# Kernel optimization log

Measured on AMD Instinct MI355X. Metric: run time of the kernel, lower is better.

The kernel has to match this reference:

```python
import jax, jax.numpy as jnp
import numpy as np

B, D, L, H, T = 256, 512, 8, 8, 71
DH = D // H
SCALE = 0.01

def _lrelu(x):
    return jax.nn.leaky_relu(x, 0.2)

def _rms(x, dims, w):
    return w * x * jax.lax.rsqrt(jnp.mean(x * x, axis=dims, keepdims=True) + 1e-6)

def _conv(x, w, b, pad):
    y = jax.lax.conv_general_dilated(x, w, (1, 1), pad, dimension_numbers=('NCHW', 'OIHW', 'NCHW'))
    return y + b[None, :, None, None]

def _mha(x, qkv, nw):
    b_, d_, t_ = x.shape
    # einsum 'bdt,nhdD->nbhtD' -> (3,B,H,T,dh)
    y = jnp.einsum('bdt,nhdD->nbhtD', _lrelu(x), qkv)
    y = _rms(y, -2, nw)  # RMSNorm over the token axis (torch dim=-2)
    q, k, v = y[0], y[1], y[2]
    attn = jax.nn.softmax(jnp.einsum('bhtd,bhTd->bhtT', q, k) / np.float32(np.sqrt(DH)), axis=-1)
    out = jnp.einsum('bhtT,bhTd->bhdt', attn, v)  # (B,H,dh,T)
    return out.reshape(b_, d_, t_)

def _convblock(x, w1, b1, w2, b2, nw):
    b_, d_, t_ = x.shape
    y = x.reshape(b_, d_, 8, 8)
    y = _conv(_lrelu(y), w1, b1, 'SAME')
    y = _rms(y, (-1, -2), nw)
    y = _conv(_lrelu(y), w2, b2, 'SAME')
    return y.reshape(b_, d_, t_)

def _forward(fen, move, rank_emb, file_emb, fen_emb, move_emb, abs_emb, ln_w, ln_b, emb_qkv, emb_norm_w, qkv, mha_norm_w, conv1_w, conv1_b, conv2_w, conv2_b, cb_norm_w, out_norm_w, co1_w, co1_b, co2_w, co2_b):
    pos = (rank_emb + file_emb).reshape(64, D)
    mv = (pos[move] + move_emb) * 0.58          # (B,2,D)
    f = fen_emb[fen]                             # (B,133,D)
    board = 0.5 * (f[:, :64] + f[:, 64:128] + pos)
    x = jnp.concatenate([board, f[:, 128:], mv], axis=1) + abs_emb  # (B,71,D)
    x = jnp.swapaxes(x, -1, -2)                  # (B,D,71)
    mu = jnp.mean(x, -1, keepdims=True)
    var = jnp.mean((x - mu) ** 2, -1, keepdims=True)
    x = (x - mu) * jax.lax.rsqrt(var + 1e-5) * ln_w + ln_b  # LayerNorm over T=71
    y = _mha(x, emb_qkv, emb_norm_w)
    x = x[:, :, :64] + y[:, :, :64]              # keep the 64 board squares
    for i in range(L):
        x = x + _convblock(x, conv1_w[i], conv1_b[i], conv2_w[i], conv2_b[i], cb_norm_w[i])
        x = x + _mha(x, qkv[i], mha_norm_w[i])
    x = x.reshape(B, D, 8, 8)
    x = _conv(_lrelu(x), co1_w, co1_b, 'SAME')
    x = _rms(x, (-1, -2), out_norm_w)
    x = _conv(_lrelu(x), co2_w, co2_b, 'VALID')  # (B,1,1,1)
    return x.reshape(-1)

def setup_inputs():
    key = jax.random.key(0)
    ks = jax.random.split(key, 16)
    n = lambda k, s, sc: jax.random.normal(k, s, dtype=jnp.float32) * sc
    return {
        'fen': jax.random.randint(ks[0], (B, 133), 0, 17),
        'move': jax.random.randint(ks[1], (B, 2), 0, 64),
        'rank_emb': n(ks[2], (8, 1, D), SCALE),
        'file_emb': n(ks[3], (1, 8, D), SCALE),
        'fen_emb': n(ks[4], (17, D), SCALE),
        'move_emb': n(ks[5], (2, D), SCALE),
        'abs_emb': n(ks[6], (71, D), SCALE),
        'ln_w': jnp.ones((71,), jnp.float32),
        'ln_b': jnp.zeros((71,), jnp.float32),
        'emb_qkv': n(ks[7], (3, H, D, DH), SCALE),
        'emb_norm_w': jnp.ones((1,), jnp.float32),
        'qkv': n(ks[8], (L, 3, H, D, DH), SCALE * 0.64),
        'mha_norm_w': jnp.ones((L, 1), jnp.float32),
        'conv1_w': n(ks[9], (L, D, D, 3, 3), SCALE * 0.64),
        'conv1_b': jnp.zeros((L, D), jnp.float32),
        'conv2_w': n(ks[10], (L, D, D, 3, 3), SCALE * 0.64),
        'conv2_b': jnp.zeros((L, D), jnp.float32),
        'cb_norm_w': jnp.ones((L, 1), jnp.float32),
        'out_norm_w': jnp.ones((1,), jnp.float32),
        'co1_w': n(ks[11], (2 * D, D, 3, 3), SCALE),
        'co1_b': jnp.zeros((2 * D,), jnp.float32),
        'co2_w': n(ks[12], (1, 2 * D, 8, 8), SCALE),
        'co2_b': jnp.zeros((1,), jnp.float32),
    }

def reference(fen, move, rank_emb, file_emb, fen_emb, move_emb, abs_emb, ln_w, ln_b, emb_qkv, emb_norm_w, qkv, mha_norm_w, conv1_w, conv1_b, conv2_w, conv2_b, cb_norm_w, out_norm_w, co1_w, co1_b, co2_w, co2_b):
    return _forward(fen, move, rank_emb, file_emb, fen_emb, move_emb, abs_emb, ln_w, ln_b, emb_qkv, emb_norm_w, qkv, mha_norm_w, conv1_w, conv1_b, conv2_w, conv2_b, cb_norm_w, out_norm_w, co1_w, co1_b, co2_w, co2_b)
```

## Files before the change

kernel.cpp:

```cpp
#include <hip/hip_runtime.h>
#include <hip/hip_bf16.h>
#include <cstdint>
#include <cstddef>


typedef float f32x4 __attribute__((ext_vector_type(4)));
typedef short short8 __attribute__((ext_vector_type(8)));

__device__ __forceinline__ float lrelu(float v) { return v > 0.f ? v : 0.2f * v; }
__device__ __forceinline__ __hip_bfloat16 tobf(float v) { return __float2bfloat16(v); }
__device__ __forceinline__ float frombf(__hip_bfloat16 v) { return __bfloat162float(v); }

__global__ __launch_bounds__(256) void repack_qkv_w0(
    const float* __restrict__ emb_qkv, __hip_bfloat16* __restrict__ Wq0)
{
  int o = blockIdx.x * 256 + threadIdx.x;
  int j = o >> 9, d = o & 511;
  int n = j >> 9, h = (j >> 6) & 7, dh = j & 63;
  Wq0[o] = tobf(emb_qkv[(((n * 8 + h) * 512 + d) << 6) + dh]);
}

__global__ __launch_bounds__(256) void repack_qkv_w2(
    const float* __restrict__ qkvw, __hip_bfloat16* __restrict__ Wq2)
{
  const int t = blockIdx.x * 256 + threadIdx.x;
  const int lane = t & 63;
  const int nj = (t >> 6) % 96;
  int rest = (t >> 6) / 96;
  const int ks = rest & 1;
  const int kc = (rest >> 1) & 7;
  const int L = rest >> 4;
  const int j = nj * 16 + (lane & 15);
  const int d0 = kc * 64 + ks * 32 + (lane >> 4) * 8;
  const int n = j >> 9, h = (j >> 6) & 7, dh = j & 63;
  const float* src = qkvw + ((((size_t)L * 3 + n) * 8 + h) * 512 + d0) * 64 + dh;
  __hip_bfloat16 tmp[8];
  #pragma unroll
  for (int e = 0; e < 8; ++e) tmp[e] = tobf(src[(size_t)e * 64]);
  *(uint4*)&Wq2[(size_t)t * 8] = *(const uint4*)tmp;
}

__global__ __launch_bounds__(256) void repack_conv_w2(
    const float* __restrict__ w, __hip_bfloat16* __restrict__ W2, int COUT)
{
  const int t = blockIdx.x * 256 + threadIdx.x;
  if (t >= (COUT << 6)) return;
  const int lr = t & 15;
  const int cbg = (t >> 4) & 63;
  const int oj = t >> 10;
  const int cc = cbg >> 3, ks = (cbg >> 2) & 1, lg = cbg & 3;
  const int o = oj * 16 + lr;
  const int NJ = COUT >> 4;
  const float* src = w + ((size_t)o * 512 + cbg * 8) * 9;
  #pragma unroll
  for (int k = 0; k < 9; ++k) {
    __hip_bfloat16 tmp[8];
    #pragma unroll
    for (int e = 0; e < 8; ++e) tmp[e] = tobf(src[e * 9 + k]);
    size_t di = ((((size_t)cc * 9 + k) * NJ + oj) * 2 + ks) * 512 + (lg * 16 + lr) * 8;
    *(uint4*)&W2[di] = *(const uint4*)tmp;
  }
}

__global__ __launch_bounds__(256) void repack_conv_pair(
    const float* __restrict__ w1, const float* __restrict__ w2s,
    __hip_bfloat16* __restrict__ WA, __hip_bfloat16* __restrict__ WB)
{
  int t = blockIdx.x * 256 + threadIdx.x;
  const float* w = (t < 32768) ? w1 : w2s;
  __hip_bfloat16* W2 = (t < 32768) ? WA : WB;
  t &= 32767;
  const int lr = t & 15;
  const int cbg = (t >> 4) & 63;
  const int oj = t >> 10;
  const int cc = cbg >> 3, ks = (cbg >> 2) & 1, lg = cbg & 3;
  const int o = oj * 16 + lr;
  const float* src = w + ((size_t)o * 512 + cbg * 8) * 9;
  #pragma unroll
  for (int k = 0; k < 9; ++k) {
    __hip_bfloat16 tmp[8];
    #pragma unroll
    for (int e = 0; e < 8; ++e) tmp[e] = tobf(src[e * 9 + k]);
    size_t di = ((((size_t)cc * 9 + k) * 32 + oj) * 2 + ks) * 512 + (lg * 16 + lr) * 8;
    *(uint4*)&W2[di] = *(const uint4*)tmp;
  }
}

__global__ __launch_bounds__(256) void build_ln_kernel(
    const int* __restrict__ fen, const int* __restrict__ move,
    const float* __restrict__ rank_emb, const float* __restrict__ file_emb,
    const float* __restrict__ fen_emb, const float* __restrict__ move_emb,
    const float* __restrict__ abs_emb, const float* __restrict__ lnw,
    const float* __restrict__ lnb, __hip_bfloat16* __restrict__ X71)
{
  const int gid = blockIdx.x * 256 + threadIdx.x;
  const int b = gid >> 9, d = gid & 511;
  const int* fb = fen + b * 133;

  float sum = 0.f, sq = 0.f, mu = 0.f, rstd = 0.f;
  #pragma unroll 1
  for (int pass = 0; pass < 2; ++pass) {
    if (pass) {
      mu = sum * (1.f / 71.f);
      float var = sq * (1.f / 71.f) - mu * mu;
      rstd = rsqrtf(var + 1e-5f);
    }
    #pragma unroll 1
    for (int t = 0; t < 71; ++t) {
      float a = abs_emb[t * 512 + d];
      float v;
      if (t < 64) {
        float pos = rank_emb[(t >> 3) * 512 + d] + file_emb[(t & 7) * 512 + d];
        v = 0.5f * (fen_emb[fb[t] * 512 + d] + fen_emb[fb[64 + t] * 512 + d] + pos) + a;
      } else if (t < 69) {
        v = fen_emb[fb[t + 64] * 512 + d] + a;
      } else {
        int j = t - 69;
        int s = move[b * 2 + j];
        float pos = rank_emb[(s >> 3) * 512 + d] + file_emb[(s & 7) * 512 + d];
        v = (pos + move_emb[j * 512 + d]) * 0.58f + a;
      }
      if (pass) X71[(size_t)gid * 71 + t] = tobf((v - mu) * rstd * lnw[t] + lnb[t]);
      else { sum += v; sq += v * v; }
    }
  }
}

template <int T, int TP>
__global__ __launch_bounds__(256) void proj71_kernel(
    const __hip_bfloat16* __restrict__ xin, const __hip_bfloat16* __restrict__ Wq,
    const float* __restrict__ nw,
    __hip_bfloat16* __restrict__ qk, __hip_bfloat16* __restrict__ vT)
{
  const int b  = blockIdx.x / 6;
  const int jb = (blockIdx.x % 6) * 256;
  const int tid = threadIdx.x;
  const int lane = tid & 63, wv = tid >> 6;
  const int lr = lane & 15, lg = lane >> 4;

  __shared__ __hip_bfloat16 xt[TP * 72];
  __shared__ __hip_bfloat16 wl[256 * 72];

  constexpr int MI = TP / 16;
  f32x4 acc[MI][4];
  #pragma unroll
  for (int mi = 0; mi < MI; ++mi)
    #pragma unroll
    for (int ni = 0; ni < 4; ++ni) acc[mi][ni] = {0.f, 0.f, 0.f, 0.f};

  for (int c0 = 0; c0 < 512; c0 += 64) {
    for (int i = tid; i < 64 * TP; i += 256) {
      int d = i / TP, t = i - d * TP;
      float v = (t < T) ? lrelu(frombf(xin[((size_t)(b * 512 + c0 + d)) * T + t])) : 0.f;
      xt[t * 72 + d] = tobf(v);
    }
    for (int i = tid; i < 2048; i += 256) {
      int j = i >> 3, cb = i & 7;
      *(uint4*)&wl[j * 72 + cb * 8] =
          *(const uint4*)&Wq[(size_t)(jb + j) * 512 + c0 + cb * 8];
    }
    __syncthreads();
    #pragma unroll
    for (int ks = 0; ks < 2; ++ks) {
      short8 a[MI], bb[4];
      #pragma unroll
      for (int mi = 0; mi < MI; ++mi)
        a[mi] = *(const short8*)&xt[(mi * 16 + lr) * 72 + ks * 32 + lg * 8];
      #pragma unroll
      for (int ni = 0; ni < 4; ++ni)
        bb[ni] = *(const short8*)&wl[(wv * 64 + ni * 16 + lr) * 72 + ks * 32 + lg * 8];
      #pragma unroll
      for (int mi = 0; mi < MI; ++mi)
        #pragma unroll
        for (int ni = 0; ni < 4; ++ni)
          acc[mi][ni] = __builtin_amdgcn_mfma_f32_16x16x32_bf16(
              a[mi], bb[ni], acc[mi][ni], 0, 0, 0);
    }
    __syncthreads();
  }

  #pragma unroll
  for (int ni = 0; ni < 4; ++ni) {
    const int j = jb + wv * 64 + ni * 16 + lr;
    float ss = 0.f;
    #pragma unroll
    for (int mi = 0; mi < MI; ++mi)
      #pragma unroll
      for (int r = 0; r < 4; ++r) ss += acc[mi][ni][r] * acc[mi][ni][r];
    ss += __shfl_xor(ss, 16);
    ss += __shfl_xor(ss, 32);
    const float sc = nw[0] * rsqrtf(ss * (1.f / T) + 1e-6f);
    if (j < 1024) {
      #pragma unroll
      for (int mi = 0; mi < MI; ++mi)
        #pragma unroll
        for (int r = 0; r < 4; ++r) {
          int t = mi * 16 + lg * 4 + r;
          if (t < T)
            qk[((size_t)b * T + t) * 1024 + j] = tobf(acc[mi][ni][r] * sc);
        }
    } else {
      const int jj = j - 1024;
      #pragma unroll
      for (int mi = 0; mi < MI; ++mi)
        #pragma unroll
        for (int r = 0; r < 4; ++r) {
          int t = mi * 16 + lg * 4 + r;
          vT[((size_t)b * 512 + jj) * TP + t] = tobf(acc[mi][ni][r] * sc);
        }
    }
  }
}

__global__ __launch_bounds__(256) void proj64_kernel(
    const float* __restrict__ x,
    const __hip_bfloat16* __restrict__ Wq2,
    const float* __restrict__ nw,
    __hip_bfloat16* __restrict__ qk, __hip_bfloat16* __restrict__ vT)
{
  const int b    = blockIdx.x / 6;
  const int jseg = blockIdx.x % 6;
  const int tid = threadIdx.x;
  const int lane = tid & 63, wv = tid >> 6;
  const int lr = lane & 15, lg = lane >> 4;

  __shared__ __hip_bfloat16 xt[2][64 * 72];

  f32x4 acc[4][4];
  #pragma unroll
  for (int mi = 0; mi < 4; ++mi)
    #pragma unroll
    for (int ni = 0; ni < 4; ++ni) acc[mi][ni] = {0.f, 0.f, 0.f, 0.f};

  f32x4 sreg[4];
  const int s_d  = tid >> 4;
  const int s_t4 = (tid & 15) << 2;

  #define PSTAGE_LOAD(kc_)                                                    \
    {                                                                         \
      const float* xb_ = x + ((size_t)b * 512 + (kc_) * 64 + s_d) * 64 + s_t4; \
      _Pragma("unroll")                                                       \
      for (int u = 0; u < 4; ++u) sreg[u] = *(const f32x4*)&xb_[u * 1024];    \
    }
  #define PSTAGE_WRITE(buf_)                                                  \
    {                                                                         \
      _Pragma("unroll")                                                       \
      for (int u = 0; u < 4; ++u) {                                           \
        _Pragma("unroll")                                                     \
        for (int j = 0; j < 4; ++j)                                           \
          xt[buf_][(s_t4 + j) * 72 + s_d + u * 16] = tobf(lrelu(sreg[u][j])); \
      }                                                                       \
    }

  PSTAGE_LOAD(0);
  PSTAGE_WRITE(0);
  __syncthreads();

  const int njb0 = jseg * 16 + wv * 4;

  for (int kc = 0; kc < 8; ++kc) {
    const int cur = kc & 1;
    if (kc < 7) PSTAGE_LOAD(kc + 1);
    const __hip_bfloat16* xb = xt[cur];
    #pragma unroll
    for (int ks = 0; ks < 2; ++ks) {
      short8 bv[4], av[4];
      #pragma unroll
      for (int ni = 0; ni < 4; ++ni)
        bv[ni] = *(const short8*)
            &Wq2[((((size_t)kc * 2 + ks) * 96) + njb0 + ni) * 512 + lane * 8];
      #pragma unroll
      for (int mi = 0; mi < 4; ++mi)
        av[mi] = *(const short8*)&xb[(mi * 16 + lr) * 72 + ks * 32 + lg * 8];
      #pragma unroll
      for (int mi = 0; mi < 4; ++mi)
        #pragma unroll
        for (int ni = 0; ni < 4; ++ni)
          acc[mi][ni] = __builtin_amdgcn_mfma_f32_16x16x32_bf16(
              av[mi], bv[ni], acc[mi][ni], 0, 0, 0);
    }
    if (kc < 7) PSTAGE_WRITE(cur ^ 1);
    __syncthreads();
  }
  #undef PSTAGE_LOAD
  #undef PSTAGE_WRITE

  #pragma unroll
  for (int ni = 0; ni < 4; ++ni) {
    const int j = jseg * 256 + wv * 64 + ni * 16 + lr;
    float ss = 0.f;
    #pragma unroll
    for (int mi = 0; mi < 4; ++mi)
      #pragma unroll
      for (int r = 0; r < 4; ++r) ss += acc[mi][ni][r] * acc[mi][ni][r];
    ss += __shfl_xor(ss, 16);
    ss += __shfl_xor(ss, 32);
    const float sc = nw[0] * rsqrtf(ss * (1.f / 64.f) + 1e-6f);
    if (j < 1024) {
      #pragma unroll
      for (int mi = 0; mi < 4; ++mi)
        #pragma unroll
        for (int r = 0; r < 4; ++r) {
          int t = mi * 16 + lg * 4 + r;
          qk[((size_t)b * 64 + t) * 1024 + j] = tobf(acc[mi][ni][r] * sc);
        }
    } else {
      const int jj = j - 1024;
      #pragma unroll
      for (int mi = 0; mi < 4; ++mi)
        #pragma unroll
        for (int r = 0; r < 4; ++r) {
          int t = mi * 16 + lg * 4 + r;
          vT[((size_t)b * 512 + jj) * 64 + t] = tobf(acc[mi][ni][r] * sc);
        }
    }
  }
}

template <int T, bool RESBF, bool WRITEXC>
__global__ __launch_bounds__(256) void attn2_kernel(
    const __hip_bfloat16* __restrict__ qk,
    const __hip_bfloat16* __restrict__ vT,
    const void* __restrict__ res, float* __restrict__ out,
    __hip_bfloat16* __restrict__ xcout)
{
  constexpr int TP = (T == 71) ? 80 : 64;
  constexpr int TK = (T + 31) / 32;
  constexpr int RS = 72;
  constexpr int PS = TK * 32 + 8;
  constexpr int KR = (T == 71) ? 80 : 64;
  constexpr int SC = (T == 71) ? 82 : 66;
  constexpr int NCF = KR / 16;
  constexpr int NFW = (NCF + 3) / 4;
  constexpr int RANGE = (TK * 32) / 4;

  constexpr int Q_OFF = 0;
  constexpr int K_OFF = Q_OFF + 64 * RS * 2;
  constexpr int V_OFF = K_OFF + KR * RS * 2;
  constexpr int S_OFF = V_OFF + 64 * PS * 2;
  constexpr int BYTES = S_OFF + 64 * SC * 4;
  __shared__ __align__(16) char smem[BYTES];
  __hip_bfloat16* qs = (__hip_bfloat16*)(smem + Q_OFF);
  __hip_bfloat16* ksh = (__hip_bfloat16*)(smem + K_OFF);
  __hip_bfloat16* vs = (__hip_bfloat16*)(smem + V_OFF);
  float* ss = (float*)(smem + S_OFF);
  __hip_bfloat16* ps = (__hip_bfloat16*)(smem + S_OFF);

  const int b = blockIdx.x >> 3, h = blockIdx.x & 7;
  const int tid = threadIdx.x;
  const int lane = tid & 63, wv = tid >> 6;
  const int lr = lane & 15, lg = lane >> 4;

  for (int i = tid; i < BYTES / 16; i += 256) ((uint4*)smem)[i] = uint4{0, 0, 0, 0};
  __syncthreads();

  const __hip_bfloat16* qb = qk + (size_t)b * T * 1024 + h * 64;
  for (int v = tid; v < 512; v += 256) {
    int t = v >> 3, d0 = (v & 7) * 8;
    *(uint4*)&qs[t * RS + d0] = *(const uint4*)&qb[(size_t)t * 1024 + d0];
  }
  for (int v = tid; v < T * 8; v += 256) {
    int t = v >> 3, d0 = (v & 7) * 8;
    *(uint4*)&ksh[t * RS + d0] = *(const uint4*)&qb[(size_t)t * 1024 + 512 + d0];
  }
  constexpr int VV = TP / 8;
  for (int v = tid; v < 64 * VV; v += 256) {
    int dh = v / VV, tc = (v - dh * VV) * 8;
    *(uint4*)&vs[dh * PS + tc] =
        *(const uint4*)&vT[((size_t)b * 512 + h * 64 + dh) * TP + tc];
  }
  __syncthreads();

  f32x4 sacc[NFW][4];
  #pragma unroll
  for (int fi = 0; fi < NFW; ++fi)
    #pragma unroll
    for (int mi = 0; mi < 4; ++mi) sacc[fi][mi] = {0.f, 0.f, 0.f, 0.f};
  #pragma unroll
  for (int ks2 = 0; ks2 < 2; ++ks2) {
    short8 a[4];
    #pragma unroll
    for (int mi = 0; mi < 4; ++mi)
      a[mi] = *(const short8*)&qs[(mi * 16 + lr) * RS + ks2 * 32 + lg * 8];
    #pragma unroll
    for (int fi = 0; fi < NFW; ++fi) {
      const int f = wv + fi * 4;
      if (f < NCF) {
        short8 bb = *(const short8*)&ksh[(f * 16 + lr) * RS + ks2 * 32 + lg * 8];
        #pragma unroll
        for (int mi = 0; mi < 4; ++mi)
          sacc[fi][mi] = __builtin_amdgcn_mfma_f32_16x16x32_bf16(
              a[mi], bb, sacc[fi][mi], 0, 0, 0);
      }
    }
  }
  #pragma unroll
  for (int fi = 0; fi < NFW; ++fi) {
    const int f = wv + fi * 4;
    if (f < NCF) {
      #pragma unroll
      for (int mi = 0; mi < 4; ++mi)
        #pragma unroll
        for (int r = 0; r < 4; ++r)
          ss[(mi * 16 + lg * 4 + r) * SC + f * 16 + lr] = sacc[fi][mi][r] * 0.125f;
    }
  }
  __syncthreads();

  {
    const int row = tid >> 2, q4 = tid & 3;
    float sv[RANGE];
    float mx = -3.0e38f;
    #pragma unroll
    for (int i = 0; i < RANGE; ++i) {
      int c = q4 * RANGE + i;
      sv[i] = (c < T) ? ss[row * SC + c] : -3.0e38f;
      mx = fmaxf(mx, sv[i]);
    }
    mx = fmaxf(mx, __shfl_xor(mx, 1));
    mx = fmaxf(mx, __shfl_xor(mx, 2));
    float sm = 0.f;
    #pragma unroll
    for (int i = 0; i < RANGE; ++i) {
      int c = q4 * RANGE + i;
      sv[i] = (c < T) ? __expf(sv[i] - mx) : 0.f;
      sm += sv[i];
    }
    sm += __shfl_xor(sm, 1);
    sm += __shfl_xor(sm, 2);
    const float inv = 1.f / sm;
    __syncthreads();
    #pragma unroll
    for (int i = 0; i < RANGE; ++i)
      ps[row * PS + q4 * RANGE + i] = tobf(sv[i] * inv);
  }
  __syncthreads();

  f32x4 oacc[4];
  #pragma unroll
  for (int mi = 0; mi < 4; ++mi) oacc[mi] = {0.f, 0.f, 0.f, 0.f};
  #pragma unroll
  for (int ks2 = 0; ks2 < TK; ++ks2) {
    short8 bb = *(const short8*)&vs[(wv * 16 + lr) * PS + ks2 * 32 + lg * 8];
    #pragma unroll
    for (int mi = 0; mi < 4; ++mi) {
      short8 a = *(const short8*)&ps[(mi * 16 + lr) * PS + ks2 * 32 + lg * 8];
      oacc[mi] = __builtin_amdgcn_mfma_f32_16x16x32_bf16(a, bb, oacc[mi], 0, 0, 0);
    }
  }

  const int dh = wv * 16 + lr;
  const size_t chb = (size_t)b * 512 + h * 64 + dh;
  #pragma unroll
  for (int mi = 0; mi < 4; ++mi) {
    const int t0 = mi * 16 + lg * 4;
    const size_t idx = chb * 64 + t0;
    f32x4 v = oacc[mi];
    if constexpr (RESBF) {
      const __hip_bfloat16* rb = (const __hip_bfloat16*)res + chb * T + t0;
      #pragma unroll
      for (int r = 0; r < 4; ++r) v[r] += frombf(rb[r]);
    } else {
      v += *(const f32x4*)&((const float*)res)[idx];
    }
    *(f32x4*)&out[idx] = v;
    if constexpr (WRITEXC) {
      #pragma unroll
      for (int r = 0; r < 4; ++r)
        xcout[((size_t)b * 64 + t0 + r) * 512 + (h << 6) + dh] = tobf(lrelu(v[r]));
    }
  }
}

template <bool RMSOUT, bool RESADD, bool INBF, bool OUTBF>
__global__ __launch_bounds__(256) void conv_mfma2b(
    const void* __restrict__ xin,
    const __hip_bfloat16* __restrict__ W2,
    const float* __restrict__ bias,
    const float* __restrict__ nw,
    const float* __restrict__ res,
    void* __restrict__ outp,
    int COUT)
{
  const int ntc = COUT >> 8;
  const int b = blockIdx.x / ntc;
  const int nt = blockIdx.x - b * ntc;
  const int o0 = nt << 8;
  const int NJ = COUT >> 4;
  const int tid = threadIdx.x;
  const int lane = tid & 63, wv = tid >> 6;
  const int lr = lane & 15, lg = lane >> 4;

  __shared__ __hip_bfloat16 xt[2][100 * 72];

  f32x4 acc[4][4];
  #pragma unroll
  for (int mi = 0; mi < 4; ++mi)
    #pragma unroll
    for (int ni = 0; ni < 4; ++ni) acc[mi][ni] = {0.f, 0.f, 0.f, 0.f};

  for (int i = tid; i < 7200; i += 256) { xt[0][i] = tobf(0.f); xt[1][i] = tobf(0.f); }

  f32x4 sreg[4];
  const int s_ci = tid >> 4;
  const int s_p4 = (tid & 15) << 2;
  const int s_row = (((s_p4 >> 3) + 1) * 10 + (s_p4 & 7) + 1) * 72;
  uint4 sregb[2];
  const int c_cg = tid & 7;
  const int c_cell0 = tid >> 3;
  const int c_lofs0 = (((c_cell0 >> 3) + 1) * 10 + (c_cell0 & 7) + 1) * 72 + c_cg * 8;
  const int c_cell1 = c_cell0 + 32;
  const int c_lofs1 = (((c_cell1 >> 3) + 1) * 10 + (c_cell1 & 7) + 1) * 72 + c_cg * 8;

  auto stage_load = [&](int cc_) {
    if constexpr (INBF) {
      const __hip_bfloat16* xbf = (const __hip_bfloat16*)xin;
      const __hip_bfloat16* p0 =
          xbf + ((size_t)b * 64 + c_cell0) * 512 + cc_ * 64 + c_cg * 8;
      sregb[0] = *(const uint4*)p0;
      sregb[1] = *(const uint4*)(p0 + 32 * 512);
    } else {
      const float* xf = (const float*)xin;
      const float* xb_ = xf + ((size_t)b * 512 + cc_ * 64 + s_ci) * 64 + s_p4;
      #pragma unroll
      for (int u = 0; u < 4; ++u) sreg[u] = *(const f32x4*)&xb_[u * 1024];
    }
  };
  auto stage_write = [&](int buf_) {
    if constexpr (INBF) {
      *(uint4*)&xt[buf_][c_lofs0] = sregb[0];
      *(uint4*)&xt[buf_][c_lofs1] = sregb[1];
    } else {
      #pragma unroll
      for (int u = 0; u < 4; ++u)
        #pragma unroll
        for (int j = 0; j < 4; ++j)
          xt[buf_][s_row + j * 72 + s_ci + u * 16] = tobf(lrelu(sreg[u][j]));
    }
  };

  stage_load(0);
  __syncthreads();
  stage_write(0);
  __syncthreads();

  const int ojb2 = ((o0 >> 4) + wv * 4) * 2;

  for (int cc = 0; cc < 8; ++cc) {
    const int cur = cc & 1;
    if (cc < 7) stage_load(cc + 1);
    const __hip_bfloat16* xb = xt[cur];

    #pragma unroll
    for (int k = 0; k < 9; ++k) {
      const int dy = k / 3 - 1, dx = k - (k / 3) * 3 - 1;
      const int ii0 = (lr >> 3) + dy + 1;
      const int jj0 = (lr & 7) + dx + 1;
      const size_t slab = ((size_t)(cc * 9 + k) * NJ) * 2 + ojb2;
      short8 bv[2][4], av[2][4];
      #pragma unroll
      for (int ni = 0; ni < 4; ++ni)
        #pragma unroll
        for (int ks = 0; ks < 2; ++ks)
          bv[ks][ni] = *(const short8*)&W2[(slab + ni * 2 + ks) * 512 + lane * 8];
      #pragma unroll
      for (int ks = 0; ks < 2; ++ks)
        #pragma unroll
        for (int mi = 0; mi < 4; ++mi)
          av[ks][mi] = *(const short8*)&xb[((ii0 + mi * 2) * 10 + jj0) * 72 + ks * 32 + lg * 8];
      #pragma unroll
      for (int ks = 0; ks < 2; ++ks)
        #pragma unroll
        for (int mi = 0; mi < 4; ++mi)
          #pragma unroll
          for (int ni = 0; ni < 4; ++ni)
            acc[mi][ni] = __builtin_amdgcn_mfma_f32_16x16x32_bf16(
                av[ks][mi], bv[ks][ni], acc[mi][ni], 0, 0, 0);
    }
    if (cc < 7) stage_write(cur ^ 1);
    __syncthreads();
  }

  #pragma unroll
  for (int ni = 0; ni < 4; ++ni) {
    const int o = o0 + wv * 64 + ni * 16 + lr;
    const float bvs = bias[o];
    float sc = 1.f;
    if constexpr (RMSOUT) {
      float ssq = 0.f;
      #pragma unroll
      for (int mi = 0; mi < 4; ++mi)
        #pragma unroll
        for (int r = 0; r < 4; ++r) {
          float v = acc[mi][ni][r] + bvs;
          ssq += v * v;
        }
      ssq += __shfl_xor(ssq, 16);
      ssq += __shfl_xor(ssq, 32);
      sc = nw[0] * rsqrtf(ssq * (1.f / 64.f) + 1e-6f);
    }
    if constexpr (OUTBF) {
      __hip_bfloat16* tc = (__hip_bfloat16*)outp;
      #pragma unroll
      for (int mi = 0; mi < 4; ++mi)
        #pragma unroll
        for (int r = 0; r < 4; ++r) {
          int cell = mi * 16 + lg * 4 + r;
          tc[((size_t)b * 64 + cell) * COUT + o] =
              tobf(lrelu((acc[mi][ni][r] + bvs) * sc));
        }
    } else {
      float* outf = (float*)outp;
      #pragma unroll
      for (int mi = 0; mi < 4; ++mi) {
        size_t idx = ((size_t)b * COUT + o) * 64 + mi * 16 + lg * 4;
        f32x4 v;
        #pragma unroll
        for (int r = 0; r < 4; ++r) v[r] = (acc[mi][ni][r] + bvs) * sc;
        if constexpr (RESADD) v += *(const f32x4*)&res[idx];
        *(f32x4*)&outf[idx] = v;
      }
    }
  }
}

__global__ __launch_bounds__(256) void co2_kernel(
    const float* __restrict__ xf, const float* __restrict__ w,
    const float* __restrict__ cb, float* __restrict__ out)
{
  const int b = blockIdx.x, tid = threadIdx.x;
  const float* xb = xf + (size_t)b * 65536;
  float acc = 0.f;
  for (int i = tid; i < 65536; i += 256)
    acc += lrelu(xb[i]) * w[i];
  #pragma unroll
  for (int off = 32; off; off >>= 1) acc += __shfl_down(acc, off);
  __shared__ float red[4];
  if ((tid & 63) == 0) red[tid >> 6] = acc;
  __syncthreads();
  if (tid == 0) out[b] = red[0] + red[1] + red[2] + red[3] + cb[0];
}

extern "C" void kernel_launch(void* const* d_in, const int* in_sizes, int n_in,
                              void* d_out, int out_size, void* d_ws, size_t ws_size,
                              hipStream_t stream)
{
  const int*   fen        = (const int*)d_in[0];
  const int*   move       = (const int*)d_in[1];
  const float* rank_emb   = (const float*)d_in[2];
  const float* file_emb   = (const float*)d_in[3];
  const float* fen_emb    = (const float*)d_in[4];
  const float* move_emb   = (const float*)d_in[5];
  const float* abs_emb    = (const float*)d_in[6];
  const float* ln_w       = (const float*)d_in[7];
  const float* ln_b       = (const float*)d_in[8];
  const float* emb_qkv    = (const float*)d_in[9];
  const float* emb_norm_w = (const float*)d_in[10];
  const float* qkvw_in    = (const float*)d_in[11];
  const float* mha_norm_w = (const float*)d_in[12];
  const float* conv1_w    = (const float*)d_in[13];
  const float* conv1_b    = (const float*)d_in[14];
  const float* conv2_w    = (const float*)d_in[15];
  const float* conv2_b    = (const float*)d_in[16];
  const float* cb_norm_w  = (const float*)d_in[17];
  const float* out_norm_w = (const float*)d_in[18];
  const float* co1_w      = (const float*)d_in[19];
  const float* co1_b      = (const float*)d_in[20];
  const float* co2_w      = (const float*)d_in[21];
  const float* co2_b      = (const float*)d_in[22];
  float* out = (float*)d_out;

  char* base = (char*)d_ws;
  __hip_bfloat16* X71 = (__hip_bfloat16*)base;
  float* X64 = (float*)(base + 18612224);
  char* t1b  = base + 52166656;
  __hip_bfloat16* Wq0 = (__hip_bfloat16*)(base + 119275520);
  __hip_bfloat16* Wq2 = (__hip_bfloat16*)(base + 120848384);
  __hip_bfloat16* qk71 = (__hip_bfloat16*)t1b;
  __hip_bfloat16* vT71 = (__hip_bfloat16*)(t1b + 37224448);
  __hip_bfloat16* qk64 = (__hip_bfloat16*)t1b;
  __hip_bfloat16* vT64 = (__hip_bfloat16*)(t1b + 33554432);
  __hip_bfloat16* Xc   = (__hip_bfloat16*)(t1b + 50331648);
  __hip_bfloat16* Tc   = (__hip_bfloat16*)t1b;
  float* F1 = (float*)t1b;
  __hip_bfloat16* WcA = (__hip_bfloat16*)base;
  __hip_bfloat16* WcB = (__hip_bfloat16*)(base + 4718592);

  repack_qkv_w0<<<3072, 256, 0, stream>>>(emb_qkv, Wq0);
  repack_qkv_w2<<<3072, 256, 0, stream>>>(qkvw_in, Wq2);

  build_ln_kernel<<<512, 256, 0, stream>>>(fen, move, rank_emb, file_emb,
                                           fen_emb, move_emb, abs_emb,
                                           ln_w, ln_b, X71);
  proj71_kernel<71, 80><<<1536, 256, 0, stream>>>(X71, Wq0, emb_norm_w, qk71, vT71);
  attn2_kernel<71, true, false><<<2048, 256, 0, stream>>>(qk71, vT71, X71, X64,
                                                          nullptr);

  for (int l = 0; l < 8; ++l) {
    repack_conv_pair<<<256, 256, 0, stream>>>(conv1_w + (size_t)l * 512 * 512 * 9,
                                              conv2_w + (size_t)l * 512 * 512 * 9,
                                              WcA, WcB);
    if (l == 0)
      conv_mfma2b<true, false, false, true><<<512, 256, 0, stream>>>(
          X64, WcA, conv1_b + l * 512, cb_norm_w + l, nullptr, Tc, 512);
    else
      conv_mfma2b<true, false, true, true><<<512, 256, 0, stream>>>(
          Xc, WcA, conv1_b + l * 512, cb_norm_w + l, nullptr, Tc, 512);
    conv_mfma2b<false, true, true, false><<<512, 256, 0, stream>>>(
        Tc, WcB, conv2_b + l * 512, nullptr, X64, X64, 512);
    proj64_kernel<<<1536, 256, 0, stream>>>(X64, Wq2 + (size_t)l * 786432,
                                            mha_norm_w + l, qk64, vT64);
    if (l < 7)
      attn2_kernel<64, false, true><<<2048, 256, 0, stream>>>(qk64, vT64, X64,
                                                              X64, Xc);
    else
      attn2_kernel<64, false, false><<<2048, 256, 0, stream>>>(qk64, vT64, X64,
                                                               X64, nullptr);
  }

  repack_conv_w2<<<256, 256, 0, stream>>>(co1_w, WcA, 1024);
  conv_mfma2b<true, false, false, false><<<1024, 256, 0, stream>>>(
      X64, WcA, co1_b, out_norm_w, nullptr, F1, 1024);
  co2_kernel<<<256, 256, 0, stream>>>(F1, co2_w, co2_b, out);
}
```

Measured before the change: 2.647 ms.

## Share conv weight fragments across two batches per block and unify qkv repack

The conv kernel now runs 512-thread blocks where two 256-thread halves process two batch elements with the same output-channel tile. Each half keeps its own double-buffered LDS slab, and blocks are ordered so neighbouring blocks touch the same weights, which is meant to improve weight reuse in cache. The embedding qkv weights are repacked into the same MFMA-fragment layout as the layer weights in a single kernel. The embedding projection then reads B fragments straight from global memory instead of staging them through LDS. The larger blocks use twice the LDS, which may lower occupancy.

New measurement: 2.709 ms. 1.02x slower.

```diff
diff --git a/kernel.cpp b/kernel.cpp
--- a/kernel.cpp
+++ b/kernel.cpp
@@ -11,17 +11,9 @@
 __device__ __forceinline__ __hip_bfloat16 tobf(float v) { return __float2bfloat16(v); }
 __device__ __forceinline__ float frombf(__hip_bfloat16 v) { return __bfloat162float(v); }
 
-__global__ __launch_bounds__(256) void repack_qkv_w0(
-    const float* __restrict__ emb_qkv, __hip_bfloat16* __restrict__ Wq0)
-{
-  int o = blockIdx.x * 256 + threadIdx.x;
-  int j = o >> 9, d = o & 511;
-  int n = j >> 9, h = (j >> 6) & 7, dh = j & 63;
-  Wq0[o] = tobf(emb_qkv[(((n * 8 + h) * 512 + d) << 6) + dh]);
-}
-
-__global__ __launch_bounds__(256) void repack_qkv_w2(
-    const float* __restrict__ qkvw, __hip_bfloat16* __restrict__ Wq2)
+__global__ __launch_bounds__(256) void repack_qkv_all(
+    const float* __restrict__ emb_qkv, const float* __restrict__ qkvw,
+    __hip_bfloat16* __restrict__ Wq2)
 {
   const int t = blockIdx.x * 256 + threadIdx.x;
   const int lane = t & 63;
@@ -33,7 +25,9 @@
   const int j = nj * 16 + (lane & 15);
   const int d0 = kc * 64 + ks * 32 + (lane >> 4) * 8;
   const int n = j >> 9, h = (j >> 6) & 7, dh = j & 63;
-  const float* src = qkvw + ((((size_t)L * 3 + n) * 8 + h) * 512 + d0) * 64 + dh;
+  const float* src =
+      (L == 0) ? emb_qkv + (((size_t)(n * 8 + h) * 512 + d0) << 6) + dh
+               : qkvw + ((((size_t)(L - 1) * 3 + n) * 8 + h) * 512 + d0) * 64 + dh;
   __hip_bfloat16 tmp[8];
   #pragma unroll
   for (int e = 0; e < 8; ++e) tmp[e] = tobf(src[(size_t)e * 64]);
@@ -127,19 +121,19 @@
 }
 
 template <int T, int TP>
-__global__ __launch_bounds__(256) void proj71_kernel(
-    const __hip_bfloat16* __restrict__ xin, const __hip_bfloat16* __restrict__ Wq,
+__global__ __launch_bounds__(256) void proj71b_kernel(
+    const __hip_bfloat16* __restrict__ xin,
+    const __hip_bfloat16* __restrict__ Wq2,
     const float* __restrict__ nw,
     __hip_bfloat16* __restrict__ qk, __hip_bfloat16* __restrict__ vT)
 {
-  const int b  = blockIdx.x / 6;
-  const int jb = (blockIdx.x % 6) * 256;
+  const int b    = blockIdx.x / 6;
+  const int jseg = blockIdx.x % 6;
   const int tid = threadIdx.x;
   const int lane = tid & 63, wv = tid >> 6;
   const int lr = lane & 15, lg = lane >> 4;
 
   __shared__ __hip_bfloat16 xt[TP * 72];
-  __shared__ __hip_bfloat16 wl[256 * 72];
 
   constexpr int MI = TP / 16;
   f32x4 acc[MI][4];
@@ -148,40 +142,39 @@
     #pragma unroll
     for (int ni = 0; ni < 4; ++ni) acc[mi][ni] = {0.f, 0.f, 0.f, 0.f};
 
-  for (int c0 = 0; c0 < 512; c0 += 64) {
+  const int njb0 = jseg * 16 + wv * 4;
+
+  for (int kc = 0; kc < 8; ++kc) {
+    const int c0 = kc * 64;
     for (int i = tid; i < 64 * TP; i += 256) {
       int d = i / TP, t = i - d * TP;
       float v = (t < T) ? lrelu(frombf(xin[((size_t)(b * 512 + c0 + d)) * T + t])) : 0.f;
       xt[t * 72 + d] = tobf(v);
     }
-    for (int i = tid; i < 2048; i += 256) {
-      int j = i >> 3, cb = i & 7;
-      *(uint4*)&wl[j * 72 + cb * 8] =
-          *(const uint4*)&Wq[(size_t)(jb + j) * 512 + c0 + cb * 8];
-    }
     __syncthreads();
     #pragma unroll
     for (int ks = 0; ks < 2; ++ks) {
-      short8 a[MI], bb[4];
+      short8 bv[4], av[MI];
+      #pragma unroll
+      for (int ni = 0; ni < 4; ++ni)
+        bv[ni] = *(const short8*)
+            &Wq2[((((size_t)kc * 2 + ks) * 96) + njb0 + ni) * 512 + lane * 8];
       #pragma unroll
       for (int mi = 0; mi < MI; ++mi)
-        a[mi] = *(const short8*)&xt[(mi * 16 + lr) * 72 + ks * 32 + lg * 8];
-      #pragma unroll
-      for (int ni = 0; ni < 4; ++ni)
-        bb[ni] = *(const short8*)&wl[(wv * 64 + ni * 16 + lr) * 72 + ks * 32 + lg * 8];
+        av[mi] = *(const short8*)&xt[(mi * 16 + lr) * 72 + ks * 32 + lg * 8];
       #pragma unroll
       for (int mi = 0; mi < MI; ++mi)
         #pragma unroll
         for (int ni = 0; ni < 4; ++ni)
           acc[mi][ni] = __builtin_amdgcn_mfma_f32_16x16x32_bf16(
-              a[mi], bb[ni], acc[mi][ni], 0, 0, 0);
+              av[mi], bv[ni], acc[mi][ni], 0, 0, 0);
     }
     __syncthreads();
   }
 
   #pragma unroll
   for (int ni = 0; ni < 4; ++ni) {
-    const int j = jb + wv * 64 + ni * 16 + lr;
+    const int j = jseg * 256 + wv * 64 + ni * 16 + lr;
     float ss = 0.f;
     #pragma unroll
     for (int mi = 0; mi < MI; ++mi)
@@ -473,7 +466,7 @@
 }
 
 template <bool RMSOUT, bool RESADD, bool INBF, bool OUTBF>
-__global__ __launch_bounds__(256) void conv_mfma2b(
+__global__ __launch_bounds__(512) void conv_mfma2c(
     const void* __restrict__ xin,
     const __hip_bfloat16* __restrict__ W2,
     const float* __restrict__ bias,
@@ -483,15 +476,20 @@
     int COUT)
 {
   const int ntc = COUT >> 8;
-  const int b = blockIdx.x / ntc;
-  const int nt = blockIdx.x - b * ntc;
+  const int lpn = 8 / ntc;
+  const int g = blockIdx.x >> 3, s = blockIdx.x & 7;
+  const int nt = s / lpn;
+  const int bp = g * lpn + (s % lpn);
   const int o0 = nt << 8;
   const int NJ = COUT >> 4;
   const int tid = threadIdx.x;
-  const int lane = tid & 63, wv = tid >> 6;
+  const int bg = tid >> 8;
+  const int t256 = tid & 255;
+  const int b = bp * 2 + bg;
+  const int lane = tid & 63, wv = (t256 >> 6);
   const int lr = lane & 15, lg = lane >> 4;
 
-  __shared__ __hip_bfloat16 xt[2][100 * 72];
+  __shared__ __hip_bfloat16 xt[2][2][100 * 72];
 
   f32x4 acc[4][4];
   #pragma unroll
@@ -499,15 +497,15 @@
     #pragma unroll
     for (int ni = 0; ni < 4; ++ni) acc[mi][ni] = {0.f, 0.f, 0.f, 0.f};
 
-  for (int i = tid; i < 7200; i += 256) { xt[0][i] = tobf(0.f); xt[1][i] = tobf(0.f); }
+  for (int i = tid; i < 3600; i += 512) ((uint4*)xt)[i] = uint4{0, 0, 0, 0};
 
   f32x4 sreg[4];
-  const int s_ci = tid >> 4;
-  const int s_p4 = (tid & 15) << 2;
+  const int s_ci = t256 >> 4;
+  const int s_p4 = (t256 & 15) << 2;
   const int s_row = (((s_p4 >> 3) + 1) * 10 + (s_p4 & 7) + 1) * 72;
   uint4 sregb[2];
-  const int c_cg = tid & 7;
-  const int c_cell0 = tid >> 3;
+  const int c_cg = t256 & 7;
+  const int c_cell0 = t256 >> 3;
   const int c_lofs0 = (((c_cell0 >> 3) + 1) * 10 + (c_cell0 & 7) + 1) * 72 + c_cg * 8;
   const int c_cell1 = c_cell0 + 32;
   const int c_lofs1 = (((c_cell1 >> 3) + 1) * 10 + (c_cell1 & 7) + 1) * 72 + c_cg * 8;
@@ -528,14 +526,14 @@
   };
   auto stage_write = [&](int buf_) {
     if constexpr (INBF) {
-      *(uint4*)&xt[buf_][c_lofs0] = sregb[0];
-      *(uint4*)&xt[buf_][c_lofs1] = sregb[1];
+      *(uint4*)&xt[buf_][bg][c_lofs0] = sregb[0];
+      *(uint4*)&xt[buf_][bg][c_lofs1] = sregb[1];
     } else {
       #pragma unroll
       for (int u = 0; u < 4; ++u)
         #pragma unroll
         for (int j = 0; j < 4; ++j)
-          xt[buf_][s_row + j * 72 + s_ci + u * 16] = tobf(lrelu(sreg[u][j]));
+          xt[buf_][bg][s_row + j * 72 + s_ci + u * 16] = tobf(lrelu(sreg[u][j]));
     }
   };
 
@@ -549,7 +547,7 @@
   for (int cc = 0; cc < 8; ++cc) {
     const int cur = cc & 1;
     if (cc < 7) stage_load(cc + 1);
-    const __hip_bfloat16* xb = xt[cur];
+    const __hip_bfloat16* xb = xt[cur][bg];
 
     #pragma unroll
     for (int k = 0; k < 9; ++k) {
@@ -674,8 +672,7 @@
   __hip_bfloat16* X71 = (__hip_bfloat16*)base;
   float* X64 = (float*)(base + 18612224);
   char* t1b  = base + 52166656;
-  __hip_bfloat16* Wq0 = (__hip_bfloat16*)(base + 119275520);
-  __hip_bfloat16* Wq2 = (__hip_bfloat16*)(base + 120848384);
+  __hip_bfloat16* Wq2 = (__hip_bfloat16*)(base + 119275520);
   __hip_bfloat16* qk71 = (__hip_bfloat16*)t1b;
   __hip_bfloat16* vT71 = (__hip_bfloat16*)(t1b + 37224448);
   __hip_bfloat16* qk64 = (__hip_bfloat16*)t1b;
@@ -686,13 +683,13 @@
   __hip_bfloat16* WcA = (__hip_bfloat16*)base;
   __hip_bfloat16* WcB = (__hip_bfloat16*)(base + 4718592);
 
-  repack_qkv_w0<<<3072, 256, 0, stream>>>(emb_qkv, Wq0);
-  repack_qkv_w2<<<3072, 256, 0, stream>>>(qkvw_in, Wq2);
+  repack_qkv_all<<<3456, 256, 0, stream>>>(emb_qkv, qkvw_in, Wq2);
 
   build_ln_kernel<<<512, 256, 0, stream>>>(fen, move, rank_emb, file_emb,
                                            fen_emb, move_emb, abs_emb,
                                            ln_w, ln_b, X71);
-  proj71_kernel<71, 80><<<1536, 256, 0, stream>>>(X71, Wq0, emb_norm_w, qk71, vT71);
+  proj71b_kernel<71, 80><<<1536, 256, 0, stream>>>(X71, Wq2, emb_norm_w,
+                                                   qk71, vT71);
   attn2_kernel<71, true, false><<<2048, 256, 0, stream>>>(qk71, vT71, X71, X64,
                                                           nullptr);
 
@@ -701,14 +698,14 @@
                                               conv2_w + (size_t)l * 512 * 512 * 9,
                                               WcA, WcB);
     if (l == 0)
-      conv_mfma2b<true, false, false, true><<<512, 256, 0, stream>>>(
+      conv_mfma2c<true, false, false, true><<<256, 512, 0, stream>>>(
           X64, WcA, conv1_b + l * 512, cb_norm_w + l, nullptr, Tc, 512);
     else
-      conv_mfma2b<true, false, true, true><<<512, 256, 0, stream>>>(
+      conv_mfma2c<true, false, true, true><<<256, 512, 0, stream>>>(
           Xc, WcA, conv1_b + l * 512, cb_norm_w + l, nullptr, Tc, 512);
-    conv_mfma2b<false, true, true, false><<<512, 256, 0, stream>>>(
+    conv_mfma2c<false, true, true, false><<<256, 512, 0, stream>>>(
         Tc, WcB, conv2_b + l * 512, nullptr, X64, X64, 512);
-    proj64_kernel<<<1536, 256, 0, stream>>>(X64, Wq2 + (size_t)l * 786432,
+    proj64_kernel<<<1536, 256, 0, stream>>>(X64, Wq2 + (size_t)(l + 1) * 786432,
                                             mha_norm_w + l, qk64, vT64);
     if (l < 7)
       attn2_kernel<64, false, true><<<2048, 256, 0, stream>>>(qk64, vT64, X64,
@@ -719,7 +716,7 @@
   }
 
   repack_conv_w2<<<256, 256, 0, stream>>>(co1_w, WcA, 1024);
-  conv_mfma2b<true, false, false, false><<<1024, 256, 0, stream>>>(
+  conv_mfma2c<true, false, false, false><<<512, 512, 0, stream>>>(
       X64, WcA, co1_b, out_norm_w, nullptr, F1, 1024);
   co2_kernel<<<256, 256, 0, stream>>>(F1, co2_w, co2_b, out);
 }
```
